# Optimization experiments

Measured on AMD Instinct MI355X. Metric: run time of the kernel, lower is better.

## Reference

```python
import jax, jax.numpy as jnp
import numpy as np
import math


def _mixed_masks(seq_len, local_scope, num_heads, dtype=jnp.float32):
    # 4 mask groups: global (none), local band, forward (j>=i), backward (j<=i)
    i = jnp.arange(seq_len)[:, None]
    j = jnp.arange(seq_len)[None, :]
    ninf = jnp.array(-jnp.inf, dtype)
    zero = jnp.zeros((seq_len, seq_len), dtype)
    g = zero
    l = jnp.where(jnp.abs(i - j) <= local_scope, 0.0, ninf).astype(dtype)
    f = jnp.where(i > j, ninf, 0.0).astype(dtype)  # keep j >= i
    b = jnp.where(i < j, ninf, 0.0).astype(dtype)  # keep j <= i
    masks = jnp.stack([g, l, f, b], axis=0)  # [4, T, T]
    # tf.repeat(..., num_heads//4, axis=0): g,g,...,l,l,...,f,...,b,...
    return jnp.repeat(masks, num_heads // 4, axis=0)  # [H, T, T]


def setup_inputs() -> dict:
    key = jax.random.key(0)
    ks = jax.random.split(key, 6)
    B, T, D, H, dk = 2, 2048, 512, 8, 64
    return {
        "query": jax.random.normal(ks[0], (B, T, D), jnp.float32),
        "value": jax.random.normal(ks[1], (B, T, D), jnp.float32),
        "Wq": jax.random.normal(ks[2], (H, D, dk), jnp.float32) * 0.02,
        "Wk": jax.random.normal(ks[3], (H, D, dk), jnp.float32) * 0.02,
        "Wv": jax.random.normal(ks[4], (H, D, dk), jnp.float32) * 0.02,
        "Wo": jax.random.normal(ks[5], (H, dk, D), jnp.float32) * 0.02,
        "local_scope": 4,
    }


def reference(query, value, Wq, Wk, Wv, Wo, local_scope):
    B, T, D = query.shape
    H, _, dk = Wq.shape
    masks = _mixed_masks(T, local_scope, H, query.dtype)  # [H, T, T]
    # projections: 'abx,cxd->acbd'
    q = jnp.einsum('btd,hdk->bhtk', query, Wq)
    k = jnp.einsum('bsd,hdk->bhsk', value, Wk)  # key defaults to value
    v = jnp.einsum('bsd,hdk->bhsk', value, Wv)
    scores = jnp.einsum('bhtk,bhsk->bhts', q, k) / math.sqrt(dk)
    scores = scores + masks[None]  # broadcast over batch
    # Keras Softmax(axis=[-1,-2]): joint softmax over both last axes
    probs = jax.nn.softmax(scores, axis=(-2, -1))
    att = jnp.einsum('bhts,bhsk->bhtk', probs, v)
    # output projection: 'axby,xyc->abc'
    out = jnp.einsum('bhtk,hkd->btd', att, Wo)
    return out
```

## Files before the change

### kernel.cpp

```cpp
#include <hip/hip_runtime.h>
#include <math.h>

#define T_SEQ  2048
#define D_MODEL 512
#define NH     8
#define DK     64
#define NKB    32
#define BH     16
#define HK     512
#define NCH    2
#define CHB    16
#define LOG2E  1.44269504088896340736f
#define QSCALE (0.125f * LOG2E)

typedef unsigned int uint;
typedef unsigned short ushort;
typedef __attribute__((ext_vector_type(8))) short bf16x8;
typedef __attribute__((ext_vector_type(4))) float f32x4;

#define QHI_B   (0ull)
#define QLO_B   (QHI_B + 4194304ull)
#define KHI_B   (QLO_B + 4194304ull)
#define KLO_B   (KHI_B + 4194304ull)
#define VTHI_B  (KLO_B + 4194304ull)
#define VTLO_B  (VTHI_B + 4194304ull)
#define WTHI_B  (VTLO_B + 4194304ull)
#define WTLO_B  (WTHI_B + 1572864ull)
#define WOTHI_B (WTLO_B + 1572864ull)
#define WOTLO_B (WOTHI_B + 524288ull)
#define ATTP_B  (WOTLO_B + 524288ull)
#define CHUNK_F 2097152ull
#define MST_B   (ATTP_B + (ull_t)NCH * 8388608ull)
#define LST_B   (MST_B + 262144ull)
#define SST_B   (LST_B + 262144ull)
#define ATTSHI_B (SST_B + 262144ull)
#define ATTSLO_B (ATTSHI_B + 4194304ull)
typedef unsigned long long ull_t;

static __device__ __forceinline__ void tsplit2(float a, float b, uint& hi, uint& lo) {
    uint ua = __float_as_uint(a), ub = __float_as_uint(b);
    uint ha = ua & 0xFFFF0000u, hb = ub & 0xFFFF0000u;
    hi = (ha >> 16) | hb;
    float ra = a - __uint_as_float(ha);
    float rb = b - __uint_as_float(hb);
    lo = (__float_as_uint(ra) >> 16) | (__float_as_uint(rb) & 0xFFFF0000u);
}

__global__ __launch_bounds__(256) void split_w(
    const float* __restrict__ Wq, const float* __restrict__ Wk,
    const float* __restrict__ Wv, const float* __restrict__ Wo,
    float* __restrict__ ws)
{
    uint* WTH = (uint*)((char*)ws + WTHI_B);
    uint* WTL = (uint*)((char*)ws + WTLO_B);
    uint* WOH = (uint*)((char*)ws + WOTHI_B);
    uint* WOL = (uint*)((char*)ws + WOTLO_B);
    const int gid = blockIdx.x * 256 + threadIdx.x;
    if (blockIdx.x < 1536) {
        const int d2 = gid & 255;
        const int k = (gid >> 8) & 63;
        const int h = (gid >> 14) & 7;
        const int which = gid >> 17;
        const float* W = (which == 0 ? Wq : (which == 1 ? Wk : Wv));
        const float* src = W + ((size_t)h * D_MODEL + 2 * d2) * DK + k;
        uint hi, lo;
        tsplit2(src[0], src[DK], hi, lo);
        const size_t o = (((size_t)(which * 8 + h) * 64 + k) * 512 + 2 * d2) >> 1;
        WTH[o] = hi; WTL[o] = lo;
    } else {
        const int o = gid - 1536 * 256;
        const int hk2 = o & 255;
        const int d = o >> 8;
        const float* src = Wo + (size_t)(2 * hk2) * D_MODEL + d;
        uint hi, lo;
        tsplit2(src[0], src[D_MODEL], hi, lo);
        const size_t oo = ((size_t)d * 512 + 2 * hk2) >> 1;
        WOH[oo] = hi; WOL[oo] = lo;
    }
}

__global__ __launch_bounds__(256) void proj_mfma(
    const float* __restrict__ query, const float* __restrict__ value,
    float* __restrict__ ws)
{
    const int which = blockIdx.z;
    const int bh = blockIdx.y, b = bh >> 3, h = bh & 7;
    const int t0 = blockIdx.x * 64;
    const float* X = (which == 0 ? query : value) + (size_t)b * T_SEQ * D_MODEL;
    const ushort* WtH = (const ushort*)((char*)ws + WTHI_B) + (size_t)(which * 8 + h) * 64 * 512;
    const ushort* WtL = (const ushort*)((char*)ws + WTLO_B) + (size_t)(which * 8 + h) * 64 * 512;
// ... 36 lines not shown
            const int row = m2 * 16 + lr;
            bf16x8 wh0 = *(const bf16x8*)&BsH[row][c0s];
            bf16x8 wh1 = *(const bf16x8*)&BsH[row][c1s];
            bf16x8 wl0 = *(const bf16x8*)&BsL[row][c0s];
            bf16x8 wl1 = *(const bf16x8*)&BsL[row][c1s];
            f32x4 a = acc[m2];
            if (which < 2) {
                a = __builtin_amdgcn_mfma_f32_16x16x32_bf16(wh0, xh0.v, a, 0, 0, 0);
                a = __builtin_amdgcn_mfma_f32_16x16x32_bf16(wh1, xh1.v, a, 0, 0, 0);
                a = __builtin_amdgcn_mfma_f32_16x16x32_bf16(wh0, xl0.v, a, 0, 0, 0);
                a = __builtin_amdgcn_mfma_f32_16x16x32_bf16(wh1, xl1.v, a, 0, 0, 0);
                a = __builtin_amdgcn_mfma_f32_16x16x32_bf16(wl0, xh0.v, a, 0, 0, 0);
                a = __builtin_amdgcn_mfma_f32_16x16x32_bf16(wl1, xh1.v, a, 0, 0, 0);
            } else {
                a = __builtin_amdgcn_mfma_f32_16x16x32_bf16(xh0.v, wh0, a, 0, 0, 0);
                a = __builtin_amdgcn_mfma_f32_16x16x32_bf16(xh1.v, wh1, a, 0, 0, 0);
                a = __builtin_amdgcn_mfma_f32_16x16x32_bf16(xl0.v, wh0, a, 0, 0, 0);
                a = __builtin_amdgcn_mfma_f32_16x16x32_bf16(xl1.v, wh1, a, 0, 0, 0);
                a = __builtin_amdgcn_mfma_f32_16x16x32_bf16(xh0.v, wl0, a, 0, 0, 0);
                a = __builtin_amdgcn_mfma_f32_16x16x32_bf16(xh1.v, wl1, a, 0, 0, 0);
            }
            acc[m2] = a;
        }
    }

    if (which < 2) {
        ushort* OH = (ushort*)((char*)ws + (which == 0 ? QHI_B : KHI_B)) + (size_t)bh * T_SEQ * DK;
        ushort* OL = (ushort*)((char*)ws + (which == 0 ? QLO_B : KLO_B)) + (size_t)bh * T_SEQ * DK;
        const float scl = (which == 0) ? QSCALE : 1.0f;
#pragma unroll
        for (int m2 = 0; m2 < 4; ++m2) {
            uint h0, l0, h1, l1;
            tsplit2(acc[m2][0] * scl, acc[m2][1] * scl, h0, l0);
            tsplit2(acc[m2][2] * scl, acc[m2][3] * scl, h1, l1);
            const size_t addr = (size_t)(t0 + w * 16 + lr) * DK + m2 * 16 + lg * 4;
            *(uint2*)&OH[addr] = make_uint2(h0, h1);
            *(uint2*)&OL[addr] = make_uint2(l0, l1);
        }
    } else {
        ushort* OH = (ushort*)((char*)ws + VTHI_B) + (size_t)bh * DK * T_SEQ;
        ushort* OL = (ushort*)((char*)ws + VTLO_B) + (size_t)bh * DK * T_SEQ;
#pragma unroll
        for (int n2 = 0; n2 < 4; ++n2) {
            uint h0, l0, h1, l1;
            tsplit2(acc[n2][0], acc[n2][1], h0, l0);
            tsplit2(acc[n2][2], acc[n2][3], h1, l1);
            const size_t addr = (size_t)(n2 * 16 + lr) * T_SEQ + t0 + w * 16 + lg * 4;
            *(uint2*)&OH[addr] = make_uint2(h0, h1);
            *(uint2*)&OL[addr] = make_uint2(l0, l1);
        }
    }
}

__global__ __launch_bounds__(256, 3) void attn_fwd(
    const int* __restrict__ ls_ptr, float* __restrict__ ws)
{
    const int bh = blockIdx.y, b = bh >> 3, h = bh & 7;
    const int mtype = h >> 1;
    const int row0 = blockIdx.x * 64, rb = row0 >> 6;
    const int chunk = blockIdx.z;
    const int ls = *ls_ptr;

    float* mrow = (float*)((char*)ws + MST_B) + ((size_t)chunk * BH + bh) * T_SEQ;
    float* lrow = (float*)((char*)ws + LST_B) + ((size_t)chunk * BH + bh) * T_SEQ;

    int klo = 0, khi = NKB - 1;
    if (mtype == 1) {
        int l2 = row0 - ls; if (l2 < 0) l2 = 0;
        int h2 = row0 + 63 + ls; if (h2 > T_SEQ - 1) h2 = T_SEQ - 1;
        klo = l2 >> 6; khi = h2 >> 6;
    } else if (mtype == 2) {
        klo = rb;
    } else if (mtype == 3) {
        khi = rb;
    }
    const int kb0 = klo > chunk * CHB ? klo : chunk * CHB;
    const int kb1 = khi < chunk * CHB + CHB - 1 ? khi : chunk * CHB + CHB - 1;

    const int tid = threadIdx.x;
    if (kb0 > kb1) {
        if (tid < 64) { mrow[row0 + tid] = -INFINITY; lrow[row0 + tid] = 0.f; }
        return;
    }

    const ushort* Qh_g = (const ushort*)((char*)ws + QHI_B) + (size_t)bh * T_SEQ * DK;
    const ushort* Ql_g = (const ushort*)((char*)ws + QLO_B) + (size_t)bh * T_SEQ * DK;
    const ushort* Kh_g = (const ushort*)((char*)ws + KHI_B) + (size_t)bh * T_SEQ * DK;
    const ushort* Kl_g = (const ushort*)((char*)ws + KLO_B) + (size_t)bh * T_SEQ * DK;
    const ushort* Vh_g = (const ushort*)((char*)ws + VTHI_B) + (size_t)bh * DK * T_SEQ;
    const ushort* Vl_g = (const ushort*)((char*)ws + VTLO_B) + (size_t)bh * DK * T_SEQ;
    float* attP = (float*)((char*)ws + ATTP_B) + (size_t)chunk * CHUNK_F;

    __shared__ ushort KhS[64][64], KlS[64][64];
    __shared__ ushort VhS[64][64], VlS[64][64];
    __shared__ ushort PhS[64][64], PlS[64][64];

    const int lane = tid & 63, w = tid >> 6;
    const int lr = lane & 15, lg = lane >> 4;
    const int sg = tid & 7, srow = tid >> 3;
    const int swz0 = (sg ^ (srow & 7)) * 8;
    const int c0s = (lg ^ (lr & 7)) * 8, c1s = c0s ^ 32;

    const ushort* qh = Qh_g + (size_t)(row0 + w * 16 + lr) * DK;
    const ushort* ql = Ql_g + (size_t)(row0 + w * 16 + lr) * DK;
    const bf16x8 bqh0 = *(const bf16x8*)(qh + lg * 8);
    const bf16x8 bqh1 = *(const bf16x8*)(qh + 32 + lg * 8);
    const bf16x8 bql0 = *(const bf16x8*)(ql + lg * 8);
    const bf16x8 bql1 = *(const bf16x8*)(ql + 32 + lg * 8);

    float m_i = -INFINITY, l_i = 0.f;
    f32x4 oacc[4];
#pragma unroll
    for (int i = 0; i < 4; ++i) oacc[i] = (f32x4){0.f, 0.f, 0.f, 0.f};

    uint4 kr0, kr1, kr2, kr3, vr0, vr1, vr2, vr3;
    kr0 = *(const uint4*)&Kh_g[(size_t)(kb0 * 64 + srow) * DK + sg * 8];
    kr1 = *(const uint4*)&Kh_g[(size_t)(kb0 * 64 + srow + 32) * DK + sg * 8];
    kr2 = *(const uint4*)&Kl_g[(size_t)(kb0 * 64 + srow) * DK + sg * 8];
    kr3 = *(const uint4*)&Kl_g[(size_t)(kb0 * 64 + srow + 32) * DK + sg * 8];
    vr0 = *(const uint4*)&Vh_g[(size_t)srow * T_SEQ + kb0 * 64 + sg * 8];
    vr1 = *(const uint4*)&Vh_g[(size_t)(srow + 32) * T_SEQ + kb0 * 64 + sg * 8];
    vr2 = *(const uint4*)&Vl_g[(size_t)srow * T_SEQ + kb0 * 64 + sg * 8];
    vr3 = *(const uint4*)&Vl_g[(size_t)(srow + 32) * T_SEQ + kb0 * 64 + sg * 8];

    for (int kb = kb0; kb <= kb1; ++kb) {
        __syncthreads();
        *(uint4*)&KhS[srow][swz0] = kr0; *(uint4*)&KhS[srow + 32][swz0] = kr1;
        *(uint4*)&KlS[srow][swz0] = kr2; *(uint4*)&KlS[srow + 32][swz0] = kr3;
        *(uint4*)&VhS[srow][swz0] = vr0; *(uint4*)&VhS[srow + 32][swz0] = vr1;
        *(uint4*)&VlS[srow][swz0] = vr2; *(uint4*)&VlS[srow + 32][swz0] = vr3;
        if (kb < kb1) {
            const int kn = kb + 1;
            kr0 = *(const uint4*)&Kh_g[(size_t)(kn * 64 + srow) * DK + sg * 8];
            kr1 = *(const uint4*)&Kh_g[(size_t)(kn * 64 + srow + 32) * DK + sg * 8];
            kr2 = *(const uint4*)&Kl_g[(size_t)(kn * 64 + srow) * DK + sg * 8];
            kr3 = *(const uint4*)&Kl_g[(size_t)(kn * 64 + srow + 32) * DK + sg * 8];
            vr0 = *(const uint4*)&Vh_g[(size_t)srow * T_SEQ + kn * 64 + sg * 8];
            vr1 = *(const uint4*)&Vh_g[(size_t)(srow + 32) * T_SEQ + kn * 64 + sg * 8];
            vr2 = *(const uint4*)&Vl_g[(size_t)srow * T_SEQ + kn * 64 + sg * 8];
            vr3 = *(const uint4*)&Vl_g[(size_t)(srow + 32) * T_SEQ + kn * 64 + sg * 8];
        }
        __syncthreads();

        f32x4 sacc[4];
#pragma unroll
        for (int m = 0; m < 4; ++m) {
            const int row = m * 16 + lr;
            bf16x8 ah0 = *(const bf16x8*)&KhS[row][c0s];
            bf16x8 ah1 = *(const bf16x8*)&KhS[row][c1s];
            bf16x8 al0 = *(const bf16x8*)&KlS[row][c0s];
            bf16x8 al1 = *(const bf16x8*)&KlS[row][c1s];
            f32x4 a = (f32x4){0.f, 0.f, 0.f, 0.f};
            a = __builtin_amdgcn_mfma_f32_16x16x32_bf16(ah0, bqh0, a, 0, 0, 0);
            a = __builtin_amdgcn_mfma_f32_16x16x32_bf16(ah1, bqh1, a, 0, 0, 0);
            a = __builtin_amdgcn_mfma_f32_16x16x32_bf16(ah0, bql0, a, 0, 0, 0);
            a = __builtin_amdgcn_mfma_f32_16x16x32_bf16(ah1, bql1, a, 0, 0, 0);
            a = __builtin_amdgcn_mfma_f32_16x16x32_bf16(al0, bqh0, a, 0, 0, 0);
            a = __builtin_amdgcn_mfma_f32_16x16x32_bf16(al1, bqh1, a, 0, 0, 0);
            sacc[m] = a;
        }

        const int t_glob = row0 + w * 16 + lr;
        const bool needmask = (mtype == 1) || ((mtype >= 2) && (kb == rb));
        float p[4][4];
        float vmax = -INFINITY;
#pragma unroll
        for (int m = 0; m < 4; ++m)
#pragma unroll
            for (int r = 0; r < 4; ++r) {
                float x = sacc[m][r];
                if (needmask) {
                    int s_glob = kb * 64 + m * 16 + lg * 4 + r;
                    bool keep;
                    if (mtype == 1) keep = (t_glob - s_glob <= ls) && (s_glob - t_glob <= ls);
                    else if (mtype == 2) keep = (s_glob >= t_glob);
                    else keep = (s_glob <= t_glob);
                    if (!keep) x = -INFINITY;
                }
                p[m][r] = x;
                vmax = fmaxf(vmax, x);
            }
        vmax = fmaxf(vmax, __shfl_xor(vmax, 16, 64));
        vmax = fmaxf(vmax, __shfl_xor(vmax, 32, 64));
        const float mn = fmaxf(m_i, vmax);
        float factor = 1.f, psum = 0.f;
        if (mn == -INFINITY) {
#pragma unroll
            for (int m = 0; m < 4; ++m)
#pragma unroll
                for (int r = 0; r < 4; ++r) p[m][r] = 0.f;
        } else {
            factor = exp2f(m_i - mn);
            m_i = mn;
#pragma unroll
            for (int m = 0; m < 4; ++m)
#pragma unroll
                for (int r = 0; r < 4; ++r) {
                    p[m][r] = exp2f(p[m][r] - mn);
                    psum += p[m][r];
                }
        }
        psum += __shfl_xor(psum, 16, 64);
        psum += __shfl_xor(psum, 32, 64);
        l_i = l_i * factor + psum;

#pragma unroll
        for (int m = 0; m < 4; ++m) {
            uint ph01, pl01, ph23, pl23;
            tsplit2(p[m][0], p[m][1], ph01, pl01);
            tsplit2(p[m][2], p[m][3], ph23, pl23);
            const int pg = (((m * 2 + (lg >> 1)) ^ (lr & 7)) * 8) + (lg & 1) * 4;
            *(uint2*)&PhS[w * 16 + lr][pg] = make_uint2(ph01, ph23);
            *(uint2*)&PlS[w * 16 + lr][pg] = make_uint2(pl01, pl23);
        }

        float fr[4];
#pragma unroll
        for (int r = 0; r < 4; ++r) fr[r] = __shfl(factor, lg * 4 + r, 64);
#pragma unroll
        for (int n2 = 0; n2 < 4; ++n2)
#pragma unroll
            for (int r = 0; r < 4; ++r) oacc[n2][r] *= fr[r];

        const bf16x8 aph0 = *(const bf16x8*)&PhS[w * 16 + lr][c0s];
        const bf16x8 aph1 = *(const bf16x8*)&PhS[w * 16 + lr][c1s];
        const bf16x8 apl0 = *(const bf16x8*)&PlS[w * 16 + lr][c0s];
        const bf16x8 apl1 = *(const bf16x8*)&PlS[w * 16 + lr][c1s];
#pragma unroll
        for (int n2 = 0; n2 < 4; ++n2) {
            const int row = n2 * 16 + lr;
            bf16x8 bh0 = *(const bf16x8*)&VhS[row][c0s];
            bf16x8 bh1 = *(const bf16x8*)&VhS[row][c1s];
            bf16x8 bl0 = *(const bf16x8*)&VlS[row][c0s];
            bf16x8 bl1 = *(const bf16x8*)&VlS[row][c1s];
            f32x4 a = oacc[n2];
            a = __builtin_amdgcn_mfma_f32_16x16x32_bf16(aph0, bh0, a, 0, 0, 0);
            a = __builtin_amdgcn_mfma_f32_16x16x32_bf16(aph1, bh1, a, 0, 0, 0);
            a = __builtin_amdgcn_mfma_f32_16x16x32_bf16(aph0, bl0, a, 0, 0, 0);
            a = __builtin_amdgcn_mfma_f32_16x16x32_bf16(aph1, bl1, a, 0, 0, 0);
            a = __builtin_amdgcn_mfma_f32_16x16x32_bf16(apl0, bh0, a, 0, 0, 0);
            a = __builtin_amdgcn_mfma_f32_16x16x32_bf16(apl1, bh1, a, 0, 0, 0);
            oacc[n2] = a;
        }
    }

#pragma unroll
    for (int n2 = 0; n2 < 4; ++n2)
#pragma unroll
        for (int r = 0; r < 4; ++r) {
            int t = row0 + w * 16 + lg * 4 + r;
            attP[((size_t)b * T_SEQ + t) * HK + h * DK + n2 * 16 + lr] = oacc[n2][r];
        }
    if (lg == 0) {
        mrow[row0 + w * 16 + lr] = m_i;
        lrow[row0 + w * 16 + lr] = l_i;
    }
}

__global__ __launch_bounds__(256) void softmax_stats(float* __restrict__ ws)
{
    const int bh = blockIdx.x;
    float* mbase = (float*)((char*)ws + MST_B);
    float* lbase = (float*)((char*)ws + LST_B);
    float* sbase = (float*)((char*)ws + SST_B);

    __shared__ float red[256];
    const int tid = threadIdx.x;
    const int n = NCH * T_SEQ;

    float mymax = -INFINITY;
    for (int i = tid; i < n; i += 256) {
        int c = i >> 11, t = i & 2047;
        mymax = fmaxf(mymax, mbase[((size_t)c * BH + bh) * T_SEQ + t]);
    }
    red[tid] = mymax; __syncthreads();
    for (int s = 128; s > 0; s >>= 1) {
        if (tid < s) red[tid] = fmaxf(red[tid], red[tid + s]);
        __syncthreads();
    }
    const float M = red[0]; __syncthreads();

    float mysum = 0.f;
    for (int i = tid; i < n; i += 256) {
        int c = i >> 11, t = i & 2047;
        size_t idx = ((size_t)c * BH + bh) * T_SEQ + t;
        mysum += lbase[idx] * exp2f(mbase[idx] - M);
    }
    red[tid] = mysum; __syncthreads();
    for (int s = 128; s > 0; s >>= 1) {
        if (tid < s) red[tid] += red[tid + s];
        __syncthreads();
    }
    const float Z = red[0];

    for (int i = tid; i < n; i += 256) {
        int c = i >> 11, t = i & 2047;
        size_t idx = ((size_t)c * BH + bh) * T_SEQ + t;
        sbase[idx] = exp2f(mbase[idx] - M) / Z;
    }
}

__global__ __launch_bounds__(256) void reduce_split(float* __restrict__ ws)
{
    const size_t flat = ((size_t)blockIdx.x * 256 + threadIdx.x) * 4;
    const float* attP = (const float*)((char*)ws + ATTP_B);
    const float* sc = (const float*)((char*)ws + SST_B);
    ushort* SH = (ushort*)((char*)ws + ATTSHI_B);
    ushort* SL = (ushort*)((char*)ws + ATTSLO_B);

    const int hk = (int)(flat & (HK - 1));
    const size_t bt = flat / HK;
    const int b = (int)(bt >> 11), t = (int)(bt & 2047);
    const int h = hk >> 6;

    float4 acc = make_float4(0.f, 0.f, 0.f, 0.f);
    for (int c = 0; c < NCH; ++c) {
        float4 a = *(const float4*)&attP[(size_t)c * CHUNK_F + flat];
        float s = sc[((size_t)c * BH + b * NH + h) * T_SEQ + t];
        acc.x = fmaf(a.x, s, acc.x); acc.y = fmaf(a.y, s, acc.y);
        acc.z = fmaf(a.z, s, acc.z); acc.w = fmaf(a.w, s, acc.w);
    }
    uint h0, l0, h1, l1;
    tsplit2(acc.x, acc.y, h0, l0);
    tsplit2(acc.z, acc.w, h1, l1);
    *(uint2*)&SH[flat] = make_uint2(h0, h1);
    *(uint2*)&SL[flat] = make_uint2(l0, l1);
}

__global__ __launch_bounds__(256) void out_proj_mfma(
    float* __restrict__ ws, float* __restrict__ out)
{
    const int d0 = blockIdx.x * 64;
    const int r0 = blockIdx.y * 64;
    const ushort* AH = (const ushort*)((char*)ws + ATTSHI_B);
    const ushort* AL = (const ushort*)((char*)ws + ATTSLO_B);
    const ushort* WoH = (const ushort*)((char*)ws + WOTHI_B);
    const ushort* WoL = (const ushort*)((char*)ws + WOTLO_B);

    __shared__ ushort BsH[64][64], BsL[64][64];

    const int tid = threadIdx.x, lane = tid & 63, w = tid >> 6;
    const int lr = lane & 15, lg = lane >> 4;
    const int sg = tid & 7, srow = tid >> 3;
    const int swz0 = (sg ^ (srow & 7)) * 8;
    const int c0s = (lg ^ (lr & 7)) * 8, c1s = c0s ^ 32;

    f32x4 acc[4];
#pragma unroll
    for (int i = 0; i < 4; ++i) acc[i] = (f32x4){0.f, 0.f, 0.f, 0.f};

    for (int k0 = 0; k0 < HK; k0 += 64) {
        __syncthreads();
        *(uint4*)&BsH[srow][swz0]      = *(const uint4*)&WoH[(size_t)(d0 + srow) * HK + k0 + sg * 8];
        *(uint4*)&BsH[srow + 32][swz0] = *(const uint4*)&WoH[(size_t)(d0 + srow + 32) * HK + k0 + sg * 8];
        *(uint4*)&BsL[srow][swz0]      = *(const uint4*)&WoL[(size_t)(d0 + srow) * HK + k0 + sg * 8];
        *(uint4*)&BsL[srow + 32][swz0] = *(const uint4*)&WoL[(size_t)(d0 + srow + 32) * HK + k0 + sg * 8];
        __syncthreads();

        const ushort* ar = AH + (size_t)(r0 + w * 16 + lr) * HK + k0;
        const ushort* al = AL + (size_t)(r0 + w * 16 + lr) * HK + k0;
        bf16x8 ah0 = *(const bf16x8*)(ar + lg * 8);
        bf16x8 ah1 = *(const bf16x8*)(ar + 32 + lg * 8);
        bf16x8 al0 = *(const bf16x8*)(al + lg * 8);
        bf16x8 al1 = *(const bf16x8*)(al + 32 + lg * 8);

#pragma unroll
        for (int n2 = 0; n2 < 4; ++n2) {
            const int row = n2 * 16 + lr;
            bf16x8 wh0 = *(const bf16x8*)&BsH[row][c0s];
            bf16x8 wh1 = *(const bf16x8*)&BsH[row][c1s];
            bf16x8 wl0 = *(const bf16x8*)&BsL[row][c0s];
            bf16x8 wl1 = *(const bf16x8*)&BsL[row][c1s];
            f32x4 a = acc[n2];
            a = __builtin_amdgcn_mfma_f32_16x16x32_bf16(ah0, wh0, a, 0, 0, 0);
            a = __builtin_amdgcn_mfma_f32_16x16x32_bf16(ah1, wh1, a, 0, 0, 0);
            a = __builtin_amdgcn_mfma_f32_16x16x32_bf16(ah0, wl0, a, 0, 0, 0);
            a = __builtin_amdgcn_mfma_f32_16x16x32_bf16(ah1, wl1, a, 0, 0, 0);
            a = __builtin_amdgcn_mfma_f32_16x16x32_bf16(al0, wh0, a, 0, 0, 0);
            a = __builtin_amdgcn_mfma_f32_16x16x32_bf16(al1, wh1, a, 0, 0, 0);
            acc[n2] = a;
        }
    }

#pragma unroll
    for (int n2 = 0; n2 < 4; ++n2)
#pragma unroll
        for (int i = 0; i < 4; ++i)
            out[(size_t)(r0 + w * 16 + lg * 4 + i) * D_MODEL + d0 + n2 * 16 + lr] = acc[n2][i];
}

extern "C" void kernel_launch(void* const* d_in, const int* in_sizes, int n_in,
                              void* d_out, int out_size, void* d_ws, size_t ws_size,
                              hipStream_t stream)
{
    const float* query = (const float*)d_in[0];
    const float* value = (const float*)d_in[1];
    const float* Wq = (const float*)d_in[2];
    const float* Wk = (const float*)d_in[3];
    const float* Wv = (const float*)d_in[4];
    const float* Wo = (const float*)d_in[5];
    const int* ls = (const int*)d_in[6];
    float* out = (float*)d_out;
    float* ws = (float*)d_ws;

    split_w<<<dim3(2048), 256, 0, stream>>>(Wq, Wk, Wv, Wo, ws);

    proj_mfma<<<dim3(T_SEQ / 64, BH, 3), 256, 0, stream>>>(query, value, ws);

    attn_fwd<<<dim3(T_SEQ / 64, BH, NCH), 256, 0, stream>>>(ls, ws);

    softmax_stats<<<dim3(BH), 256, 0, stream>>>(ws);

    reduce_split<<<dim3(2 * T_SEQ * HK / 1024), 256, 0, stream>>>(ws);

    out_proj_mfma<<<dim3(D_MODEL / 64, 2 * T_SEQ / 64), 256, 0, stream>>>(ws, out);
}
```

Measured before the change: 140.6 us.

## Use 32x32 MFMA tiles with 128-row query blocks in attention kernel

Rewrites the attention forward kernel so each block handles 128 query rows, with each wave covering 32 rows via 32x32x16 bf16 MFMAs instead of 16x16x32. P is rearranged into MFMA operand layout with cross-lane shuffles rather than a round trip through shared memory, and the output is staged through shared memory so the global stores are coalesced. This amortizes each K/V tile load over twice as many query rows and drops the P shared-memory buffers. In exchange it raises register pressure (occupancy hint lowered to 2), halves the grid size, and does more masked or wasted work on the causal and banded heads.

Result: slower. 185.7 us (+32.1%).

```diff
diff --git a/kernel.cpp b/kernel.cpp
--- a/kernel.cpp
+++ b/kernel.cpp
@@ -17,6 +17,7 @@
 typedef unsigned short ushort;
 typedef __attribute__((ext_vector_type(8))) short bf16x8;
 typedef __attribute__((ext_vector_type(4))) float f32x4;
+typedef __attribute__((ext_vector_type(16))) float f32x16;
 
 #define QHI_B   (0ull)
 #define QLO_B   (QHI_B + 4194304ull)
@@ -178,12 +179,13 @@
     }
 }
 
-__global__ __launch_bounds__(256, 3) void attn_fwd(
+__global__ __launch_bounds__(256, 2) void attn_fwd(
     const int* __restrict__ ls_ptr, float* __restrict__ ws)
 {
     const int bh = blockIdx.y, b = bh >> 3, h = bh & 7;
     const int mtype = h >> 1;
-    const int row0 = blockIdx.x * 64, rb = row0 >> 6;
+    const int row0 = blockIdx.x * 128;
+    const int rb = row0 >> 6;
     const int chunk = blockIdx.z;
     const int ls = *ls_ptr;
 
@@ -193,19 +195,19 @@
     int klo = 0, khi = NKB - 1;
     if (mtype == 1) {
         int l2 = row0 - ls; if (l2 < 0) l2 = 0;
-        int h2 = row0 + 63 + ls; if (h2 > T_SEQ - 1) h2 = T_SEQ - 1;
+        int h2 = row0 + 127 + ls; if (h2 > T_SEQ - 1) h2 = T_SEQ - 1;
         klo = l2 >> 6; khi = h2 >> 6;
     } else if (mtype == 2) {
         klo = rb;
     } else if (mtype == 3) {
-        khi = rb;
+        khi = rb + 1;
     }
     const int kb0 = klo > chunk * CHB ? klo : chunk * CHB;
     const int kb1 = khi < chunk * CHB + CHB - 1 ? khi : chunk * CHB + CHB - 1;
 
     const int tid = threadIdx.x;
     if (kb0 > kb1) {
-        if (tid < 64) { mrow[row0 + tid] = -INFINITY; lrow[row0 + tid] = 0.f; }
+        if (tid < 128) { mrow[row0 + tid] = -INFINITY; lrow[row0 + tid] = 0.f; }
         return;
     }
 
@@ -217,27 +219,26 @@
     const ushort* Vl_g = (const ushort*)((char*)ws + VTLO_B) + (size_t)bh * DK * T_SEQ;
     float* attP = (float*)((char*)ws + ATTP_B) + (size_t)chunk * CHUNK_F;
 
-    __shared__ ushort KhS[64][64], KlS[64][64];
-    __shared__ ushort VhS[64][64], VlS[64][64];
-    __shared__ ushort PhS[64][64], PlS[64][64];
+    __shared__ union SMem {
+        struct { ushort Kh[64][64], Kl[64][64], Vh[64][64], Vl[64][64]; } kv;
+        float ot[128][66];
+    } sm;
 
     const int lane = tid & 63, w = tid >> 6;
-    const int lr = lane & 15, lg = lane >> 4;
+    const int ln31 = lane & 31, hi5 = lane >> 5;
     const int sg = tid & 7, srow = tid >> 3;
     const int swz0 = (sg ^ (srow & 7)) * 8;
-    const int c0s = (lg ^ (lr & 7)) * 8, c1s = c0s ^ 32;
-
-    const ushort* qh = Qh_g + (size_t)(row0 + w * 16 + lr) * DK;
-    const ushort* ql = Ql_g + (size_t)(row0 + w * 16 + lr) * DK;
-    const bf16x8 bqh0 = *(const bf16x8*)(qh + lg * 8);
-    const bf16x8 bqh1 = *(const bf16x8*)(qh + 32 + lg * 8);
-    const bf16x8 bql0 = *(const bf16x8*)(ql + lg * 8);
-    const bf16x8 bql1 = *(const bf16x8*)(ql + 32 + lg * 8);
+
+    const int t_my = row0 + w * 32 + ln31;
+    bf16x8 qh[4], ql[4];
+#pragma unroll
+    for (int ks = 0; ks < 4; ++ks) {
+        qh[ks] = *(const bf16x8*)&Qh_g[(size_t)t_my * DK + ks * 16 + hi5 * 8];
+        ql[ks] = *(const bf16x8*)&Ql_g[(size_t)t_my * DK + ks * 16 + hi5 * 8];
+    }
 
     float m_i = -INFINITY, l_i = 0.f;
-    f32x4 oacc[4];
-#pragma unroll
-    for (int i = 0; i < 4; ++i) oacc[i] = (f32x4){0.f, 0.f, 0.f, 0.f};
+    f32x16 oacc0 = {}, oacc1 = {};
 
     uint4 kr0, kr1, kr2, kr3, vr0, vr1, vr2, vr3;
     kr0 = *(const uint4*)&Kh_g[(size_t)(kb0 * 64 + srow) * DK + sg * 8];
@@ -251,10 +252,10 @@
 
     for (int kb = kb0; kb <= kb1; ++kb) {
         __syncthreads();
-        *(uint4*)&KhS[srow][swz0] = kr0; *(uint4*)&KhS[srow + 32][swz0] = kr1;
-        *(uint4*)&KlS[srow][swz0] = kr2; *(uint4*)&KlS[srow + 32][swz0] = kr3;
-        *(uint4*)&VhS[srow][swz0] = vr0; *(uint4*)&VhS[srow + 32][swz0] = vr1;
-        *(uint4*)&VlS[srow][swz0] = vr2; *(uint4*)&VlS[srow + 32][swz0] = vr3;
+        *(uint4*)&sm.kv.Kh[srow][swz0] = kr0; *(uint4*)&sm.kv.Kh[srow + 32][swz0] = kr1;
+        *(uint4*)&sm.kv.Kl[srow][swz0] = kr2; *(uint4*)&sm.kv.Kl[srow + 32][swz0] = kr3;
+        *(uint4*)&sm.kv.Vh[srow][swz0] = vr0; *(uint4*)&sm.kv.Vh[srow + 32][swz0] = vr1;
+        *(uint4*)&sm.kv.Vl[srow][swz0] = vr2; *(uint4*)&sm.kv.Vl[srow + 32][swz0] = vr3;
         if (kb < kb1) {
             const int kn = kb + 1;
             kr0 = *(const uint4*)&Kh_g[(size_t)(kn * 64 + srow) * DK + sg * 8];
@@ -268,118 +269,122 @@
         }
         __syncthreads();
 
-        f32x4 sacc[4];
-#pragma unroll
-        for (int m = 0; m < 4; ++m) {
-            const int row = m * 16 + lr;
-            bf16x8 ah0 = *(const bf16x8*)&KhS[row][c0s];
-            bf16x8 ah1 = *(const bf16x8*)&KhS[row][c1s];
-            bf16x8 al0 = *(const bf16x8*)&KlS[row][c0s];
-            bf16x8 al1 = *(const bf16x8*)&KlS[row][c1s];
-            f32x4 a = (f32x4){0.f, 0.f, 0.f, 0.f};
-            a = __builtin_amdgcn_mfma_f32_16x16x32_bf16(ah0, bqh0, a, 0, 0, 0);
-            a = __builtin_amdgcn_mfma_f32_16x16x32_bf16(ah1, bqh1, a, 0, 0, 0);
-            a = __builtin_amdgcn_mfma_f32_16x16x32_bf16(ah0, bql0, a, 0, 0, 0);
-            a = __builtin_amdgcn_mfma_f32_16x16x32_bf16(ah1, bql1, a, 0, 0, 0);
-            a = __builtin_amdgcn_mfma_f32_16x16x32_bf16(al0, bqh0, a, 0, 0, 0);
-            a = __builtin_amdgcn_mfma_f32_16x16x32_bf16(al1, bqh1, a, 0, 0, 0);
-            sacc[m] = a;
-        }
-
-        const int t_glob = row0 + w * 16 + lr;
-        const bool needmask = (mtype == 1) || ((mtype >= 2) && (kb == rb));
-        float p[4][4];
+        f32x16 s0 = {}, s1 = {};
+#pragma unroll
+        for (int ks = 0; ks < 4; ++ks) {
+            const int col = (((ks * 2 + hi5) ^ (ln31 & 7)) * 8);
+            bf16x8 ah0 = *(const bf16x8*)&sm.kv.Kh[ln31][col];
+            bf16x8 al0 = *(const bf16x8*)&sm.kv.Kl[ln31][col];
+            bf16x8 ah1 = *(const bf16x8*)&sm.kv.Kh[32 + ln31][col];
+            bf16x8 al1 = *(const bf16x8*)&sm.kv.Kl[32 + ln31][col];
+            s0 = __builtin_amdgcn_mfma_f32_32x32x16_bf16(ah0, qh[ks], s0, 0, 0, 0);
+            s0 = __builtin_amdgcn_mfma_f32_32x32x16_bf16(ah0, ql[ks], s0, 0, 0, 0);
+            s0 = __builtin_amdgcn_mfma_f32_32x32x16_bf16(al0, qh[ks], s0, 0, 0, 0);
+            s1 = __builtin_amdgcn_mfma_f32_32x32x16_bf16(ah1, qh[ks], s1, 0, 0, 0);
+            s1 = __builtin_amdgcn_mfma_f32_32x32x16_bf16(ah1, ql[ks], s1, 0, 0, 0);
+            s1 = __builtin_amdgcn_mfma_f32_32x32x16_bf16(al1, qh[ks], s1, 0, 0, 0);
+        }
+
+        const bool needmask = (mtype == 1) || ((mtype >= 2) && (kb <= rb + 1));
+        float p0[16], p1[16];
         float vmax = -INFINITY;
 #pragma unroll
-        for (int m = 0; m < 4; ++m)
-#pragma unroll
-            for (int r = 0; r < 4; ++r) {
-                float x = sacc[m][r];
-                if (needmask) {
-                    int s_glob = kb * 64 + m * 16 + lg * 4 + r;
-                    bool keep;
-                    if (mtype == 1) keep = (t_glob - s_glob <= ls) && (s_glob - t_glob <= ls);
-                    else if (mtype == 2) keep = (s_glob >= t_glob);
-                    else keep = (s_glob <= t_glob);
-                    if (!keep) x = -INFINITY;
+        for (int r = 0; r < 16; ++r) {
+            float x0 = s0[r], x1 = s1[r];
+            if (needmask) {
+                const int sl = (r & 3) + 8 * (r >> 2) + 4 * hi5;
+                const int sg0 = kb * 64 + sl, sg1 = sg0 + 32;
+                bool k0, k1;
+                if (mtype == 1) {
+                    k0 = (t_my - sg0 <= ls) && (sg0 - t_my <= ls);
+                    k1 = (t_my - sg1 <= ls) && (sg1 - t_my <= ls);
+                } else if (mtype == 2) {
+                    k0 = (sg0 >= t_my); k1 = (sg1 >= t_my);
+                } else {
+                    k0 = (sg0 <= t_my); k1 = (sg1 <= t_my);
                 }
-                p[m][r] = x;
-                vmax = fmaxf(vmax, x);
+                if (!k0) x0 = -INFINITY;
+                if (!k1) x1 = -INFINITY;
             }
-        vmax = fmaxf(vmax, __shfl_xor(vmax, 16, 64));
+            p0[r] = x0; p1[r] = x1;
+            vmax = fmaxf(vmax, fmaxf(x0, x1));
+        }
         vmax = fmaxf(vmax, __shfl_xor(vmax, 32, 64));
         const float mn = fmaxf(m_i, vmax);
         float factor = 1.f, psum = 0.f;
         if (mn == -INFINITY) {
 #pragma unroll
-            for (int m = 0; m < 4; ++m)
-#pragma unroll
-                for (int r = 0; r < 4; ++r) p[m][r] = 0.f;
+            for (int r = 0; r < 16; ++r) { p0[r] = 0.f; p1[r] = 0.f; }
         } else {
             factor = exp2f(m_i - mn);
             m_i = mn;
 #pragma unroll
-            for (int m = 0; m < 4; ++m)
-#pragma unroll
-                for (int r = 0; r < 4; ++r) {
-                    p[m][r] = exp2f(p[m][r] - mn);
-                    psum += p[m][r];
-                }
-        }
-        psum += __shfl_xor(psum, 16, 64);
+            for (int r = 0; r < 16; ++r) {
+                p0[r] = exp2f(p0[r] - mn);
+                p1[r] = exp2f(p1[r] - mn);
+                psum += p0[r] + p1[r];
+            }
+        }
         psum += __shfl_xor(psum, 32, 64);
         l_i = l_i * factor + psum;
 
-#pragma unroll
-        for (int m = 0; m < 4; ++m) {
-            uint ph01, pl01, ph23, pl23;
-            tsplit2(p[m][0], p[m][1], ph01, pl01);
-            tsplit2(p[m][2], p[m][3], ph23, pl23);
-            const int pg = (((m * 2 + (lg >> 1)) ^ (lr & 7)) * 8) + (lg & 1) * 4;
-            *(uint2*)&PhS[w * 16 + lr][pg] = make_uint2(ph01, ph23);
-            *(uint2*)&PlS[w * 16 + lr][pg] = make_uint2(pl01, pl23);
-        }
-
-        float fr[4];
-#pragma unroll
-        for (int r = 0; r < 4; ++r) fr[r] = __shfl(factor, lg * 4 + r, 64);
-#pragma unroll
-        for (int n2 = 0; n2 < 4; ++n2)
-#pragma unroll
-            for (int r = 0; r < 4; ++r) oacc[n2][r] *= fr[r];
-
-        const bf16x8 aph0 = *(const bf16x8*)&PhS[w * 16 + lr][c0s];
-        const bf16x8 aph1 = *(const bf16x8*)&PhS[w * 16 + lr][c1s];
-        const bf16x8 apl0 = *(const bf16x8*)&PlS[w * 16 + lr][c0s];
-        const bf16x8 apl1 = *(const bf16x8*)&PlS[w * 16 + lr][c1s];
-#pragma unroll
-        for (int n2 = 0; n2 < 4; ++n2) {
-            const int row = n2 * 16 + lr;
-            bf16x8 bh0 = *(const bf16x8*)&VhS[row][c0s];
-            bf16x8 bh1 = *(const bf16x8*)&VhS[row][c1s];
-            bf16x8 bl0 = *(const bf16x8*)&VlS[row][c0s];
-            bf16x8 bl1 = *(const bf16x8*)&VlS[row][c1s];
-            f32x4 a = oacc[n2];
-            a = __builtin_amdgcn_mfma_f32_16x16x32_bf16(aph0, bh0, a, 0, 0, 0);
-            a = __builtin_amdgcn_mfma_f32_16x16x32_bf16(aph1, bh1, a, 0, 0, 0);
-            a = __builtin_amdgcn_mfma_f32_16x16x32_bf16(aph0, bl0, a, 0, 0, 0);
-            a = __builtin_amdgcn_mfma_f32_16x16x32_bf16(aph1, bl1, a, 0, 0, 0);
-            a = __builtin_amdgcn_mfma_f32_16x16x32_bf16(apl0, bh0, a, 0, 0, 0);
-            a = __builtin_amdgcn_mfma_f32_16x16x32_bf16(apl1, bh1, a, 0, 0, 0);
-            oacc[n2] = a;
-        }
-    }
-
-#pragma unroll
-    for (int n2 = 0; n2 < 4; ++n2)
-#pragma unroll
-        for (int r = 0; r < 4; ++r) {
-            int t = row0 + w * 16 + lg * 4 + r;
-            attP[((size_t)b * T_SEQ + t) * HK + h * DK + n2 * 16 + lr] = oacc[n2][r];
-        }
-    if (lg == 0) {
-        mrow[row0 + w * 16 + lr] = m_i;
-        lrow[row0 + w * 16 + lr] = l_i;
+        bf16x8 pfh[4], pfl[4];
+#pragma unroll
+        for (int sb = 0; sb < 4; ++sb) {
+            const float* pv = (sb < 2) ? p0 : p1;
+            const int base = (sb & 1) * 8;
+            uint oh0, oh1, oh2, oh3, ol0, ol1, ol2, ol3;
+            tsplit2(pv[base + 0], pv[base + 1], oh0, ol0);
+            tsplit2(pv[base + 2], pv[base + 3], oh1, ol1);
+            tsplit2(pv[base + 4], pv[base + 5], oh2, ol2);
+            tsplit2(pv[base + 6], pv[base + 7], oh3, ol3);
+            uint sa_h = hi5 ? oh0 : oh2, sb_h = hi5 ? oh1 : oh3;
+            uint sa_l = hi5 ? ol0 : ol2, sb_l = hi5 ? ol1 : ol3;
+            uint ra_h = __shfl_xor(sa_h, 32, 64), rb_h = __shfl_xor(sb_h, 32, 64);
+            uint ra_l = __shfl_xor(sa_l, 32, 64), rb_l = __shfl_xor(sb_l, 32, 64);
+            union { bf16x8 v; uint u[4]; } fh, fl;
+            fh.u[0] = hi5 ? ra_h : oh0; fh.u[1] = hi5 ? rb_h : oh1;
+            fh.u[2] = hi5 ? oh2 : ra_h; fh.u[3] = hi5 ? oh3 : rb_h;
+            fl.u[0] = hi5 ? ra_l : ol0; fl.u[1] = hi5 ? rb_l : ol1;
+            fl.u[2] = hi5 ? ol2 : ra_l; fl.u[3] = hi5 ? ol3 : rb_l;
+            pfh[sb] = fh.v; pfl[sb] = fl.v;
+        }
+
+        oacc0 = oacc0 * factor;
+        oacc1 = oacc1 * factor;
+
+#pragma unroll
+        for (int sb = 0; sb < 4; ++sb) {
+            const int col = (((sb * 2 + hi5) ^ (ln31 & 7)) * 8);
+            bf16x8 vh0 = *(const bf16x8*)&sm.kv.Vh[ln31][col];
+            bf16x8 vl0 = *(const bf16x8*)&sm.kv.Vl[ln31][col];
+            bf16x8 vh1 = *(const bf16x8*)&sm.kv.Vh[32 + ln31][col];
+            bf16x8 vl1 = *(const bf16x8*)&sm.kv.Vl[32 + ln31][col];
+            oacc0 = __builtin_amdgcn_mfma_f32_32x32x16_bf16(vh0, pfh[sb], oacc0, 0, 0, 0);
+            oacc0 = __builtin_amdgcn_mfma_f32_32x32x16_bf16(vh0, pfl[sb], oacc0, 0, 0, 0);
+            oacc0 = __builtin_amdgcn_mfma_f32_32x32x16_bf16(vl0, pfh[sb], oacc0, 0, 0, 0);
+            oacc1 = __builtin_amdgcn_mfma_f32_32x32x16_bf16(vh1, pfh[sb], oacc1, 0, 0, 0);
+            oacc1 = __builtin_amdgcn_mfma_f32_32x32x16_bf16(vh1, pfl[sb], oacc1, 0, 0, 0);
+            oacc1 = __builtin_amdgcn_mfma_f32_32x32x16_bf16(vl1, pfh[sb], oacc1, 0, 0, 0);
+        }
+    }
+
+    __syncthreads();
+#pragma unroll
+    for (int r = 0; r < 16; ++r) {
+        const int dk = (r & 3) + 8 * (r >> 2) + 4 * hi5;
+        sm.ot[w * 32 + ln31][dk] = oacc0[r];
+        sm.ot[w * 32 + ln31][32 + dk] = oacc1[r];
+    }
+    __syncthreads();
+#pragma unroll
+    for (int i = 0; i < 32; ++i) {
+        const int trow = w * 32 + i;
+        attP[((size_t)b * T_SEQ + row0 + trow) * HK + h * DK + lane] = sm.ot[trow][lane];
+    }
+    if (hi5 == 0) {
+        mrow[row0 + w * 32 + ln31] = m_i;
+        lrow[row0 + w * 32 + ln31] = l_i;
     }
 }
 
@@ -533,7 +538,7 @@
 
     proj_mfma<<<dim3(T_SEQ / 64, BH, 3), 256, 0, stream>>>(query, value, ws);
 
-    attn_fwd<<<dim3(T_SEQ / 64, BH, NCH), 256, 0, stream>>>(ls, ws);
+    attn_fwd<<<dim3(T_SEQ / 128, BH, NCH), 256, 0, stream>>>(ls, ws);
 
     softmax_stats<<<dim3(BH), 256, 0, stream>>>(ws);
 
```

## Process 128 query rows per attention block and use four key chunks

Applied to the files above, without the earlier changes.

Each attention block now handles 128 query rows, two 16-row fragments per wave, so every K/V tile staged in shared memory is reused across twice as many queries. To keep enough blocks in flight, the key dimension is split into four chunks when the workspace is large enough, otherwise two. The mask range and the diagonal-block masking are adjusted for the wider row tile. In exchange, each thread uses more registers (occupancy hint lowered to 2), the P tile in shared memory doubles, and the per-chunk partial outputs and stats that must be reduced afterward may grow.

Result: slower. 171.4 us (+21.9%).

```diff
diff --git a/kernel.cpp b/kernel.cpp
--- a/kernel.cpp
+++ b/kernel.cpp
@@ -8,13 +8,12 @@
 #define NKB    32
 #define BH     16
 #define HK     512
-#define NCH    2
-#define CHB    16
 #define LOG2E  1.44269504088896340736f
 #define QSCALE (0.125f * LOG2E)
 
 typedef unsigned int uint;
 typedef unsigned short ushort;
+typedef unsigned long long ull_t;
 typedef __attribute__((ext_vector_type(8))) short bf16x8;
 typedef __attribute__((ext_vector_type(4))) float f32x4;
 
@@ -30,12 +29,12 @@
 #define WOTLO_B (WOTHI_B + 524288ull)
 #define ATTP_B  (WOTLO_B + 524288ull)
 #define CHUNK_F 2097152ull
-#define MST_B   (ATTP_B + (ull_t)NCH * 8388608ull)
-#define LST_B   (MST_B + 262144ull)
-#define SST_B   (LST_B + 262144ull)
-#define ATTSHI_B (SST_B + 262144ull)
+#define MST_B   (ATTP_B + 4ull * 8388608ull)
+#define LST_B   (MST_B + 524288ull)
+#define SST_B   (LST_B + 524288ull)
+#define ATTSHI_B (SST_B + 524288ull)
 #define ATTSLO_B (ATTSHI_B + 4194304ull)
-typedef unsigned long long ull_t;
+#define WS_NEED4 (ATTSLO_B + 4194304ull)
 
 static __device__ __forceinline__ void tsplit2(float a, float b, uint& hi, uint& lo) {
     uint ua = __float_as_uint(a), ub = __float_as_uint(b);
@@ -178,12 +177,13 @@
     }
 }
 
-__global__ __launch_bounds__(256, 3) void attn_fwd(
-    const int* __restrict__ ls_ptr, float* __restrict__ ws)
+__global__ __launch_bounds__(256, 2) void attn_fwd(
+    const int* __restrict__ ls_ptr, float* __restrict__ ws, int chb, int nch)
 {
     const int bh = blockIdx.y, b = bh >> 3, h = bh & 7;
     const int mtype = h >> 1;
-    const int row0 = blockIdx.x * 64, rb = row0 >> 6;
+    const int row0 = blockIdx.x * 128;
+    const int rb = row0 >> 6;
     const int chunk = blockIdx.z;
     const int ls = *ls_ptr;
 
@@ -193,19 +193,19 @@
     int klo = 0, khi = NKB - 1;
     if (mtype == 1) {
         int l2 = row0 - ls; if (l2 < 0) l2 = 0;
-        int h2 = row0 + 63 + ls; if (h2 > T_SEQ - 1) h2 = T_SEQ - 1;
+        int h2 = row0 + 127 + ls; if (h2 > T_SEQ - 1) h2 = T_SEQ - 1;
         klo = l2 >> 6; khi = h2 >> 6;
     } else if (mtype == 2) {
         klo = rb;
     } else if (mtype == 3) {
-        khi = rb;
-    }
-    const int kb0 = klo > chunk * CHB ? klo : chunk * CHB;
-    const int kb1 = khi < chunk * CHB + CHB - 1 ? khi : chunk * CHB + CHB - 1;
+        khi = rb + 1;
+    }
+    const int kb0 = klo > chunk * chb ? klo : chunk * chb;
+    const int kb1 = khi < chunk * chb + chb - 1 ? khi : chunk * chb + chb - 1;
 
     const int tid = threadIdx.x;
     if (kb0 > kb1) {
-        if (tid < 64) { mrow[row0 + tid] = -INFINITY; lrow[row0 + tid] = 0.f; }
+        if (tid < 128) { mrow[row0 + tid] = -INFINITY; lrow[row0 + tid] = 0.f; }
         return;
     }
 
@@ -219,7 +219,7 @@
 
     __shared__ ushort KhS[64][64], KlS[64][64];
     __shared__ ushort VhS[64][64], VlS[64][64];
-    __shared__ ushort PhS[64][64], PlS[64][64];
+    __shared__ ushort PhS[128][64], PlS[128][64];
 
     const int lane = tid & 63, w = tid >> 6;
     const int lr = lane & 15, lg = lane >> 4;
@@ -227,17 +227,24 @@
     const int swz0 = (sg ^ (srow & 7)) * 8;
     const int c0s = (lg ^ (lr & 7)) * 8, c1s = c0s ^ 32;
 
-    const ushort* qh = Qh_g + (size_t)(row0 + w * 16 + lr) * DK;
-    const ushort* ql = Ql_g + (size_t)(row0 + w * 16 + lr) * DK;
-    const bf16x8 bqh0 = *(const bf16x8*)(qh + lg * 8);
-    const bf16x8 bqh1 = *(const bf16x8*)(qh + 32 + lg * 8);
-    const bf16x8 bql0 = *(const bf16x8*)(ql + lg * 8);
-    const bf16x8 bql1 = *(const bf16x8*)(ql + 32 + lg * 8);
-
-    float m_i = -INFINITY, l_i = 0.f;
-    f32x4 oacc[4];
-#pragma unroll
-    for (int i = 0; i < 4; ++i) oacc[i] = (f32x4){0.f, 0.f, 0.f, 0.f};
+    bf16x8 bqh0[2], bqh1[2], bql0[2], bql1[2];
+#pragma unroll
+    for (int tf = 0; tf < 2; ++tf) {
+        const int t = row0 + w * 32 + tf * 16 + lr;
+        const ushort* qh = Qh_g + (size_t)t * DK;
+        const ushort* ql = Ql_g + (size_t)t * DK;
+        bqh0[tf] = *(const bf16x8*)(qh + lg * 8);
+        bqh1[tf] = *(const bf16x8*)(qh + 32 + lg * 8);
+        bql0[tf] = *(const bf16x8*)(ql + lg * 8);
+        bql1[tf] = *(const bf16x8*)(ql + 32 + lg * 8);
+    }
+
+    float m_i[2] = {-INFINITY, -INFINITY}, l_i[2] = {0.f, 0.f};
+    f32x4 oacc[2][4];
+#pragma unroll
+    for (int tf = 0; tf < 2; ++tf)
+#pragma unroll
+        for (int i = 0; i < 4; ++i) oacc[tf][i] = (f32x4){0.f, 0.f, 0.f, 0.f};
 
     uint4 kr0, kr1, kr2, kr3, vr0, vr1, vr2, vr3;
     kr0 = *(const uint4*)&Kh_g[(size_t)(kb0 * 64 + srow) * DK + sg * 8];
@@ -268,7 +275,11 @@
         }
         __syncthreads();
 
-        f32x4 sacc[4];
+        f32x4 sacc[2][4];
+#pragma unroll
+        for (int tf = 0; tf < 2; ++tf)
+#pragma unroll
+            for (int m = 0; m < 4; ++m) sacc[tf][m] = (f32x4){0.f, 0.f, 0.f, 0.f};
 #pragma unroll
         for (int m = 0; m < 4; ++m) {
             const int row = m * 16 + lr;
@@ -276,82 +287,94 @@
             bf16x8 ah1 = *(const bf16x8*)&KhS[row][c1s];
             bf16x8 al0 = *(const bf16x8*)&KlS[row][c0s];
             bf16x8 al1 = *(const bf16x8*)&KlS[row][c1s];
-            f32x4 a = (f32x4){0.f, 0.f, 0.f, 0.f};
-            a = __builtin_amdgcn_mfma_f32_16x16x32_bf16(ah0, bqh0, a, 0, 0, 0);
-            a = __builtin_amdgcn_mfma_f32_16x16x32_bf16(ah1, bqh1, a, 0, 0, 0);
-            a = __builtin_amdgcn_mfma_f32_16x16x32_bf16(ah0, bql0, a, 0, 0, 0);
-            a = __builtin_amdgcn_mfma_f32_16x16x32_bf16(ah1, bql1, a, 0, 0, 0);
-            a = __builtin_amdgcn_mfma_f32_16x16x32_bf16(al0, bqh0, a, 0, 0, 0);
-            a = __builtin_amdgcn_mfma_f32_16x16x32_bf16(al1, bqh1, a, 0, 0, 0);
-            sacc[m] = a;
-        }
-
-        const int t_glob = row0 + w * 16 + lr;
-        const bool needmask = (mtype == 1) || ((mtype >= 2) && (kb == rb));
-        float p[4][4];
-        float vmax = -INFINITY;
-#pragma unroll
-        for (int m = 0; m < 4; ++m)
-#pragma unroll
-            for (int r = 0; r < 4; ++r) {
-                float x = sacc[m][r];
-                if (needmask) {
-                    int s_glob = kb * 64 + m * 16 + lg * 4 + r;
-                    bool keep;
-                    if (mtype == 1) keep = (t_glob - s_glob <= ls) && (s_glob - t_glob <= ls);
-                    else if (mtype == 2) keep = (s_glob >= t_glob);
-                    else keep = (s_glob <= t_glob);
-                    if (!keep) x = -INFINITY;
+#pragma unroll
+            for (int tf = 0; tf < 2; ++tf) {
+                f32x4 a = sacc[tf][m];
+                a = __builtin_amdgcn_mfma_f32_16x16x32_bf16(ah0, bqh0[tf], a, 0, 0, 0);
+                a = __builtin_amdgcn_mfma_f32_16x16x32_bf16(ah1, bqh1[tf], a, 0, 0, 0);
+                a = __builtin_amdgcn_mfma_f32_16x16x32_bf16(ah0, bql0[tf], a, 0, 0, 0);
+                a = __builtin_amdgcn_mfma_f32_16x16x32_bf16(ah1, bql1[tf], a, 0, 0, 0);
+                a = __builtin_amdgcn_mfma_f32_16x16x32_bf16(al0, bqh0[tf], a, 0, 0, 0);
+                a = __builtin_amdgcn_mfma_f32_16x16x32_bf16(al1, bqh1[tf], a, 0, 0, 0);
+                sacc[tf][m] = a;
+            }
+        }
+
+        const bool needmask = (mtype == 1) || ((mtype >= 2) && (kb <= rb + 1));
+#pragma unroll
+        for (int tf = 0; tf < 2; ++tf) {
+            const int t_my = row0 + w * 32 + tf * 16 + lr;
+            float p[4][4];
+            float vmax = -INFINITY;
+#pragma unroll
+            for (int m = 0; m < 4; ++m)
+#pragma unroll
+                for (int r = 0; r < 4; ++r) {
+                    float x = sacc[tf][m][r];
+                    if (needmask) {
+                        int s_glob = kb * 64 + m * 16 + lg * 4 + r;
+                        bool keep;
+                        if (mtype == 1) keep = (t_my - s_glob <= ls) && (s_glob - t_my <= ls);
+                        else if (mtype == 2) keep = (s_glob >= t_my);
+                        else keep = (s_glob <= t_my);
+                        if (!keep) x = -INFINITY;
+                    }
+                    p[m][r] = x;
+                    vmax = fmaxf(vmax, x);
                 }
-                p[m][r] = x;
-                vmax = fmaxf(vmax, x);
+            vmax = fmaxf(vmax, __shfl_xor(vmax, 16, 64));
+            vmax = fmaxf(vmax, __shfl_xor(vmax, 32, 64));
+            const float mn = fmaxf(m_i[tf], vmax);
+            float factor = 1.f, psum = 0.f;
+            if (mn == -INFINITY) {
+#pragma unroll
+                for (int m = 0; m < 4; ++m)
+#pragma unroll
+                    for (int r = 0; r < 4; ++r) p[m][r] = 0.f;
+            } else {
+                factor = exp2f(m_i[tf] - mn);
+                m_i[tf] = mn;
+#pragma unroll
+                for (int m = 0; m < 4; ++m)
+#pragma unroll
+                    for (int r = 0; r < 4; ++r) {
+                        p[m][r] = exp2f(p[m][r] - mn);
+                        psum += p[m][r];
+                    }
             }
-        vmax = fmaxf(vmax, __shfl_xor(vmax, 16, 64));
-        vmax = fmaxf(vmax, __shfl_xor(vmax, 32, 64));
-        const float mn = fmaxf(m_i, vmax);
-        float factor = 1.f, psum = 0.f;
-        if (mn == -INFINITY) {
-#pragma unroll
-            for (int m = 0; m < 4; ++m)
-#pragma unroll
-                for (int r = 0; r < 4; ++r) p[m][r] = 0.f;
-        } else {
-            factor = exp2f(m_i - mn);
-            m_i = mn;
-#pragma unroll
-            for (int m = 0; m < 4; ++m)
-#pragma unroll
-                for (int r = 0; r < 4; ++r) {
-                    p[m][r] = exp2f(p[m][r] - mn);
-                    psum += p[m][r];
-                }
-        }
-        psum += __shfl_xor(psum, 16, 64);
-        psum += __shfl_xor(psum, 32, 64);
-        l_i = l_i * factor + psum;
-
-#pragma unroll
-        for (int m = 0; m < 4; ++m) {
-            uint ph01, pl01, ph23, pl23;
-            tsplit2(p[m][0], p[m][1], ph01, pl01);
-            tsplit2(p[m][2], p[m][3], ph23, pl23);
-            const int pg = (((m * 2 + (lg >> 1)) ^ (lr & 7)) * 8) + (lg & 1) * 4;
-            *(uint2*)&PhS[w * 16 + lr][pg] = make_uint2(ph01, ph23);
-            *(uint2*)&PlS[w * 16 + lr][pg] = make_uint2(pl01, pl23);
-        }
-
-        float fr[4];
-#pragma unroll
-        for (int r = 0; r < 4; ++r) fr[r] = __shfl(factor, lg * 4 + r, 64);
-#pragma unroll
-        for (int n2 = 0; n2 < 4; ++n2)
-#pragma unroll
-            for (int r = 0; r < 4; ++r) oacc[n2][r] *= fr[r];
-
-        const bf16x8 aph0 = *(const bf16x8*)&PhS[w * 16 + lr][c0s];
-        const bf16x8 aph1 = *(const bf16x8*)&PhS[w * 16 + lr][c1s];
-        const bf16x8 apl0 = *(const bf16x8*)&PlS[w * 16 + lr][c0s];
-        const bf16x8 apl1 = *(const bf16x8*)&PlS[w * 16 + lr][c1s];
+            psum += __shfl_xor(psum, 16, 64);
+            psum += __shfl_xor(psum, 32, 64);
+            l_i[tf] = l_i[tf] * factor + psum;
+
+            const int prow = w * 32 + tf * 16 + lr;
+#pragma unroll
+            for (int m = 0; m < 4; ++m) {
+                uint ph01, pl01, ph23, pl23;
+                tsplit2(p[m][0], p[m][1], ph01, pl01);
+                tsplit2(p[m][2], p[m][3], ph23, pl23);
+                const int pg = (((m * 2 + (lg >> 1)) ^ (lr & 7)) * 8) + (lg & 1) * 4;
+                *(uint2*)&PhS[prow][pg] = make_uint2(ph01, ph23);
+                *(uint2*)&PlS[prow][pg] = make_uint2(pl01, pl23);
+            }
+
+            float fr[4];
+#pragma unroll
+            for (int r = 0; r < 4; ++r) fr[r] = __shfl(factor, lg * 4 + r, 64);
+#pragma unroll
+            for (int n2 = 0; n2 < 4; ++n2)
+#pragma unroll
+                for (int r = 0; r < 4; ++r) oacc[tf][n2][r] *= fr[r];
+        }
+
+        bf16x8 aph0[2], aph1[2], apl0[2], apl1[2];
+#pragma unroll
+        for (int tf = 0; tf < 2; ++tf) {
+            const int prow = w * 32 + tf * 16 + lr;
+            aph0[tf] = *(const bf16x8*)&PhS[prow][c0s];
+            aph1[tf] = *(const bf16x8*)&PhS[prow][c1s];
+            apl0[tf] = *(const bf16x8*)&PlS[prow][c0s];
+            apl1[tf] = *(const bf16x8*)&PlS[prow][c1s];
+        }
 #pragma unroll
         for (int n2 = 0; n2 < 4; ++n2) {
             const int row = n2 * 16 + lr;
@@ -359,31 +382,39 @@
             bf16x8 bh1 = *(const bf16x8*)&VhS[row][c1s];
             bf16x8 bl0 = *(const bf16x8*)&VlS[row][c0s];
             bf16x8 bl1 = *(const bf16x8*)&VlS[row][c1s];
-            f32x4 a = oacc[n2];
-            a = __builtin_amdgcn_mfma_f32_16x16x32_bf16(aph0, bh0, a, 0, 0, 0);
-            a = __builtin_amdgcn_mfma_f32_16x16x32_bf16(aph1, bh1, a, 0, 0, 0);
-            a = __builtin_amdgcn_mfma_f32_16x16x32_bf16(aph0, bl0, a, 0, 0, 0);
-            a = __builtin_amdgcn_mfma_f32_16x16x32_bf16(aph1, bl1, a, 0, 0, 0);
-            a = __builtin_amdgcn_mfma_f32_16x16x32_bf16(apl0, bh0, a, 0, 0, 0);
-            a = __builtin_amdgcn_mfma_f32_16x16x32_bf16(apl1, bh1, a, 0, 0, 0);
-            oacc[n2] = a;
-        }
-    }
-
-#pragma unroll
-    for (int n2 = 0; n2 < 4; ++n2)
-#pragma unroll
-        for (int r = 0; r < 4; ++r) {
-            int t = row0 + w * 16 + lg * 4 + r;
-            attP[((size_t)b * T_SEQ + t) * HK + h * DK + n2 * 16 + lr] = oacc[n2][r];
-        }
+#pragma unroll
+            for (int tf = 0; tf < 2; ++tf) {
+                f32x4 a = oacc[tf][n2];
+                a = __builtin_amdgcn_mfma_f32_16x16x32_bf16(aph0[tf], bh0, a, 0, 0, 0);
+                a = __builtin_amdgcn_mfma_f32_16x16x32_bf16(aph1[tf], bh1, a, 0, 0, 0);
+                a = __builtin_amdgcn_mfma_f32_16x16x32_bf16(aph0[tf], bl0, a, 0, 0, 0);
+                a = __builtin_amdgcn_mfma_f32_16x16x32_bf16(aph1[tf], bl1, a, 0, 0, 0);
+                a = __builtin_amdgcn_mfma_f32_16x16x32_bf16(apl0[tf], bh0, a, 0, 0, 0);
+                a = __builtin_amdgcn_mfma_f32_16x16x32_bf16(apl1[tf], bh1, a, 0, 0, 0);
+                oacc[tf][n2] = a;
+            }
+        }
+    }
+
+#pragma unroll
+    for (int tf = 0; tf < 2; ++tf)
+#pragma unroll
+        for (int n2 = 0; n2 < 4; ++n2)
+#pragma unroll
+            for (int r = 0; r < 4; ++r) {
+                int t = row0 + w * 32 + tf * 16 + lg * 4 + r;
+                attP[((size_t)b * T_SEQ + t) * HK + h * DK + n2 * 16 + lr] = oacc[tf][n2][r];
+            }
     if (lg == 0) {
-        mrow[row0 + w * 16 + lr] = m_i;
-        lrow[row0 + w * 16 + lr] = l_i;
-    }
-}
-
-__global__ __launch_bounds__(256) void softmax_stats(float* __restrict__ ws)
+#pragma unroll
+        for (int tf = 0; tf < 2; ++tf) {
+            mrow[row0 + w * 32 + tf * 16 + lr] = m_i[tf];
+            lrow[row0 + w * 32 + tf * 16 + lr] = l_i[tf];
+        }
+    }
+}
+
+__global__ __launch_bounds__(256) void softmax_stats(float* __restrict__ ws, int nch)
 {
     const int bh = blockIdx.x;
     float* mbase = (float*)((char*)ws + MST_B);
@@ -392,7 +423,7 @@
 
     __shared__ float red[256];
     const int tid = threadIdx.x;
-    const int n = NCH * T_SEQ;
+    const int n = nch * T_SEQ;
 
     float mymax = -INFINITY;
     for (int i = tid; i < n; i += 256) {
@@ -426,7 +457,7 @@
     }
 }
 
-__global__ __launch_bounds__(256) void reduce_split(float* __restrict__ ws)
+__global__ __launch_bounds__(256) void reduce_split(float* __restrict__ ws, int nch)
 {
     const size_t flat = ((size_t)blockIdx.x * 256 + threadIdx.x) * 4;
     const float* attP = (const float*)((char*)ws + ATTP_B);
@@ -440,7 +471,7 @@
     const int h = hk >> 6;
 
     float4 acc = make_float4(0.f, 0.f, 0.f, 0.f);
-    for (int c = 0; c < NCH; ++c) {
+    for (int c = 0; c < nch; ++c) {
         float4 a = *(const float4*)&attP[(size_t)c * CHUNK_F + flat];
         float s = sc[((size_t)c * BH + b * NH + h) * T_SEQ + t];
         acc.x = fmaf(a.x, s, acc.x); acc.y = fmaf(a.y, s, acc.y);
@@ -529,15 +560,18 @@
     float* out = (float*)d_out;
     float* ws = (float*)d_ws;
 
+    const int nch = (ws_size >= (size_t)WS_NEED4) ? 4 : 2;
+    const int chb = NKB / nch;
+
     split_w<<<dim3(2048), 256, 0, stream>>>(Wq, Wk, Wv, Wo, ws);
 
     proj_mfma<<<dim3(T_SEQ / 64, BH, 3), 256, 0, stream>>>(query, value, ws);
 
-    attn_fwd<<<dim3(T_SEQ / 64, BH, NCH), 256, 0, stream>>>(ls, ws);
-
-    softmax_stats<<<dim3(BH), 256, 0, stream>>>(ws);
-
-    reduce_split<<<dim3(2 * T_SEQ * HK / 1024), 256, 0, stream>>>(ws);
+    attn_fwd<<<dim3(T_SEQ / 128, BH, nch), 256, 0, stream>>>(ls, ws, chb, nch);
+
+    softmax_stats<<<dim3(BH), 256, 0, stream>>>(ws, nch);
+
+    reduce_split<<<dim3(2 * T_SEQ * HK / 1024), 256, 0, stream>>>(ws, nch);
 
     out_proj_mfma<<<dim3(D_MODEL / 64, 2 * T_SEQ / 64), 256, 0, stream>>>(ws, out);
 }
```
